# Kernel tuning notes

Measured on AMD Instinct MI355X. Metric: run time of the kernel, lower is better.

Reference implementation:

```python
import jax, jax.numpy as jnp
import numpy as np
from jax.scipy.linalg import solve_triangular

OMEGA = 1.5  # params_fix['omega']
BS, N, MAXITER = 512, 256, 200
RTOL = 1e-6


def setup_inputs() -> dict:
    key = jax.random.key(0)
    k1, k2, k3 = jax.random.split(key, 3)
    # diagonally dominant A so SOR converges
    A = jax.random.normal(k1, (BS, N, N), jnp.float32) + N * jnp.eye(N, dtype=jnp.float32)
    b = jax.random.normal(k2, (BS, N), jnp.float32)
    x_sol = jnp.linalg.solve(A, b[..., None])[..., 0]
    theta = jax.random.normal(k3, (BS, N), jnp.float32)  # initial iterate x0
    rtol = jnp.full((BS,), RTOL, jnp.float32)
    return {"A": A, "b": b, "x_sol": x_sol, "theta": theta, "rtol": rtol, "maxiter": MAXITER}


def reference(A, b, x_sol, theta, rtol, maxiter):
    bs, n, _ = A.shape
    b = b.reshape(bs, n, 1)
    x0 = theta.reshape(bs, n, 1)
    xs = x_sol.reshape(bs, n, 1)

    diag = jnp.diagonal(A, axis1=1, axis2=2)          # [bs, n]
    D = jnp.eye(n, dtype=A.dtype) * diag[:, :, None]  # diag_embed
    L = jnp.tril(A, -1)
    U = jnp.triu(A, 1)

    omega = jnp.asarray(OMEGA, A.dtype)
    G1 = D + omega * L                      # lower triangular, [bs, n, n]
    G2 = omega * U + (omega - 1.0) * D
    G = solve_triangular(G1, -G2, lower=True)        # iteration matrix
    f = solve_triangular(G1, omega * b, lower=True)  # affine term

    err0 = jnp.linalg.norm(xs - x0, axis=(1, 2))     # [bs]
    xtol = jnp.linalg.norm(xs, axis=(1, 2)) * rtol   # [bs]

    def step(carry, _):
        x, err, done = carry
        # global stopping criterion: while any(err > xtol)
        done = jnp.logical_or(done, jnp.logical_not(jnp.any(err > xtol)))
        x_new = jnp.where(done, x, G @ x + f)
        err_new = jnp.where(done, err, jnp.linalg.norm(xs - x_new, axis=(1, 2)))
        hist = jnp.where(done, jnp.zeros_like(err), err_new)  # unwritten slots stay 0
        return (x_new, err_new, done), hist

    init = (x0, err0, jnp.asarray(False))
    _, hist = jax.lax.scan(step, init, None, length=maxiter)  # hist: [maxiter, bs]
    return jnp.concatenate([err0[:, None], hist.T], axis=1)   # [bs, maxiter+1]
```

## Files before the change

kernel.cpp:

```cpp
#include <hip/hip_runtime.h>
#include <math.h>

#define BS 512
#define NN 256
#define RB 16
#define OMEGA_F 1.5f

__global__ __launch_bounds__(1024, 4) void sor_precompute(
    const float* __restrict__ A,
    const float* __restrict__ xs,
    const float* __restrict__ x0,
    const float* __restrict__ rtol,
    const int* __restrict__ maxiter_p,
    float* __restrict__ Gt,
    float* __restrict__ e0,
    float* __restrict__ err0_a,
    float* __restrict__ xtol_a,
    float* __restrict__ out)
{
    const int b   = blockIdx.x;
    const int tid = threadIdx.x;
    const int t   = tid & 255;
    const int q   = tid >> 8;
    const float* __restrict__ Ab  = A  + (size_t)b * NN * NN;
    float* __restrict__       Gtb = Gt + (size_t)b * NN * NN;

    __shared__ __align__(16) char smem[65536];
    float (*ldsA)[NN]     = (float (*)[NN])(smem);
    float (*acc2)[RB][NN] = (float (*)[RB][NN])(smem + 16384);
    float (*xbuf)[NN]     = (float (*)[NN])(smem + 49152);
    float* rs             = (float*)(smem + 16384);

    const int mi = *maxiter_p;

    if (q == 0) {
        const float xsv = xs[b * NN + t];
        const float ev  = xsv - x0[b * NN + t];
        e0[b * NN + t] = ev;
        float s1 = ev * ev, s2 = xsv * xsv;
        #pragma unroll
        for (int off = 32; off > 0; off >>= 1) {
            s1 += __shfl_down(s1, off);
            s2 += __shfl_down(s2, off);
        }
        if ((t & 63) == 0) { rs[t >> 6] = s1; rs[4 + (t >> 6)] = s2; }
    }
    __syncthreads();
    if (tid == 0) {
        const float S1 = rs[0] + rs[1] + rs[2] + rs[3];
        const float S2 = rs[4] + rs[5] + rs[6] + rs[7];
        const float er0 = sqrtf(S1);
        err0_a[b] = er0;
        xtol_a[b] = sqrtf(S2) * rtol[b];
        out[(size_t)b * (mi + 1)] = er0;
    }

    float g[4][RB];

    for (int KB = 0; KB < NN / RB; ++KB) {
        const int r0 = KB * RB;
        __syncthreads();
        {
            const int rr = tid >> 6;
            const int c  = (tid & 63) << 2;
            *(float4*)&ldsA[rr][c] = *(const float4*)&Ab[(size_t)(r0 + rr) * NN + c];
        }
        __syncthreads();

        float acc[RB];
        #pragma unroll
        for (int rr = 0; rr < RB; ++rr) acc[rr] = 0.f;
        #pragma unroll
        for (int m = 0; m < 4; ++m) {
            const int kbj = 4 * m + q;
            if (kbj < KB) {
                const int j0 = kbj * RB;
                #pragma unroll
                for (int jj4 = 0; jj4 < RB / 4; ++jj4) {
                    const float g0 = g[m][4 * jj4 + 0];
                    const float g1 = g[m][4 * jj4 + 1];
                    const float g2 = g[m][4 * jj4 + 2];
                    const float g3 = g[m][4 * jj4 + 3];
                    #pragma unroll
                    for (int rr = 0; rr < RB; ++rr) {
                        const float4 a4 = *(const float4*)&ldsA[rr][j0 + 4 * jj4];
                        acc[rr] += a4.x * g0 + a4.y * g1 + a4.z * g2 + a4.w * g3;
                    }
                }
            }
        }
        if (q < 2) {
            #pragma unroll
            for (int rr = 0; rr < RB; ++rr) acc2[q][rr][t] = acc[rr];
        }
        __syncthreads();
        if (q >= 2) {
            #pragma unroll
            for (int rr = 0; rr < RB; ++rr) acc2[q - 2][rr][t] += acc[rr];
        }
        __syncthreads();

        if (q == 0) {
            float s_[RB];
            #pragma unroll
            for (int rr = 0; rr < RB; ++rr)
                s_[rr] = acc2[0][rr][t] + acc2[1][rr][t];
            #pragma unroll
            for (int rr = 0; rr < RB; ++rr) {
                const int r = r0 + rr;
                const float a_rt = ldsA[rr][t];
                const float brt  = (t > r) ? (-OMEGA_F) * a_rt
                                 : ((t == r) ? (1.0f - OMEGA_F) * a_rt : 0.0f);
                const float diag = ldsA[rr][r];
                const float val  = (brt - OMEGA_F * s_[rr]) / diag;
                xbuf[rr][t] = val;
                Gtb[(size_t)t * NN + r] = val;
                #pragma unroll
                for (int rr2 = rr + 1; rr2 < RB; ++rr2)
                    s_[rr2] += ldsA[rr2][r] * val;
            }
        }
        __syncthreads();
        #pragma unroll
        for (int m = 0; m < 4; ++m) {
            if ((KB >> 2) == m && (KB & 3) == q) {
                #pragma unroll
                for (int rr = 0; rr < RB; ++rr) g[m][rr] = xbuf[rr][t];
            }
        }
    }
}

__global__ __launch_bounds__(1024, 4) void sor_iterate(
    const float* __restrict__ Gt,
    const float* __restrict__ e0,
    const float* __restrict__ err0_a,
    const float* __restrict__ xtol_a,
    const int* __restrict__ maxiter_p,
    float* __restrict__ out)
{
    const int b   = blockIdx.x;
    const int tid = threadIdx.x;
    const int w   = tid >> 6, u = tid & 63;
    const float* __restrict__ Gtb = Gt + (size_t)b * NN * NN;

    __shared__ __align__(16) float  e[NN];
    __shared__ __align__(16) float4 buf[16][64];
    __shared__ float errs_s;

    float4 g[16];
    #pragma unroll
    for (int jj = 0; jj < 16; ++jj)
        g[jj] = *(const float4*)&Gtb[(size_t)(16 * w + jj) * NN + 4 * u];

    if (tid < NN) e[tid] = e0[b * NN + tid];
    float err = err0_a[b];
    const float xtol = xtol_a[b];
    const int mi = *maxiter_p;
    float* __restrict__ outb = out + (size_t)b * (mi + 1);
    __syncthreads();

    int s = 1;
    for (; s <= mi; ++s) {
        if (!(err > xtol)) break;
        float4 acc = make_float4(0.f, 0.f, 0.f, 0.f);
        #pragma unroll
        for (int m = 0; m < 4; ++m) {
            const float4 ev = *(const float4*)&e[16 * w + 4 * m];
            acc.x += g[4*m+0].x*ev.x + g[4*m+1].x*ev.y + g[4*m+2].x*ev.z + g[4*m+3].x*ev.w;
            acc.y += g[4*m+0].y*ev.x + g[4*m+1].y*ev.y + g[4*m+2].y*ev.z + g[4*m+3].y*ev.w;
            acc.z += g[4*m+0].z*ev.x + g[4*m+1].z*ev.y + g[4*m+2].z*ev.z + g[4*m+3].z*ev.w;
            acc.w += g[4*m+0].w*ev.x + g[4*m+1].w*ev.y + g[4*m+2].w*ev.z + g[4*m+3].w*ev.w;
        }
        buf[w][u] = acc;
        __syncthreads();
        float4 p;
        if (w < 4) {
            const float4 p1 = buf[w + 4][u], p2 = buf[w + 8][u], p3 = buf[w + 12][u];
            p.x = acc.x + p1.x + p2.x + p3.x;
            p.y = acc.y + p1.y + p2.y + p3.y;
            p.z = acc.z + p1.z + p2.z + p3.z;
            p.w = acc.w + p1.w + p2.w + p3.w;
            if (w) buf[w][u] = p;
        }
        __syncthreads();
        if (w == 0) {
            const float4 b1 = buf[1][u], b2 = buf[2][u], b3 = buf[3][u];
            float4 r;
            r.x = p.x + b1.x + b2.x + b3.x;
            r.y = p.y + b1.y + b2.y + b3.y;
            r.z = p.z + b1.z + b2.z + b3.z;
            r.w = p.w + b1.w + b2.w + b3.w;
            *(float4*)&e[4 * u] = r;
            float loc = r.x * r.x + r.y * r.y + r.z * r.z + r.w * r.w;
            #pragma unroll
            for (int off = 32; off > 0; off >>= 1) loc += __shfl_down(loc, off);
            if (u == 0) {
                const float er = sqrtf(loc);
                errs_s = er;
                outb[s] = er;
            }
        }
        __syncthreads();
        err = errs_s;
    }
    for (int idx = s + tid; idx <= mi; idx += 1024) outb[idx] = 0.f;
}

extern "C" void kernel_launch(void* const* d_in, const int* in_sizes, int n_in,
                              void* d_out, int out_size, void* d_ws, size_t ws_size,
                              hipStream_t stream) {
    const float* A     = (const float*)d_in[0];
    const float* xs    = (const float*)d_in[2];
    const float* theta = (const float*)d_in[3];
    const float* rtol  = (const float*)d_in[4];
    const int*   mi    = (const int*)d_in[5];
    float* out = (float*)d_out;

    float* Gt   = (float*)d_ws;
    float* e0   = Gt + (size_t)BS * NN * NN;
    float* err0 = e0 + (size_t)BS * NN;
    float* xtol = err0 + BS;

    sor_precompute<<<dim3(BS), dim3(1024), 0, stream>>>(
        A, xs, theta, rtol, mi, Gt, e0, err0, xtol, out);
    sor_iterate<<<dim3(BS), dim3(1024), 0, stream>>>(
        Gt, e0, err0, xtol, mi, out);
}
```

Baseline: 661.0 us.

## Fuse SOR precompute and iteration kernels, keeping iteration matrix in registers

Merges the triangular-solve precompute and the SOR iteration loop into one kernel. The iteration matrix G is redistributed from the solve's register layout into the iteration layout through a skewed LDS transpose, so it is never written to or read back from global memory. The inner triangular-solve product now reads A directly from global/L1 instead of the LDS tile, and the wave-uniform branch index is forced scalar with readfirstlane. This removes a launch and a large global round trip of G, at the cost of register pressure, extra LDS transposes and possibly slower direct global reads of A.

```diff
diff --git a/kernel.cpp b/kernel.cpp
--- a/kernel.cpp
+++ b/kernel.cpp
@@ -6,37 +6,40 @@
 #define RB 16
 #define OMEGA_F 1.5f
 
-__global__ __launch_bounds__(1024, 4) void sor_precompute(
+__global__ __launch_bounds__(1024, 4) void sor_fused(
     const float* __restrict__ A,
     const float* __restrict__ xs,
     const float* __restrict__ x0,
     const float* __restrict__ rtol,
     const int* __restrict__ maxiter_p,
-    float* __restrict__ Gt,
-    float* __restrict__ e0,
-    float* __restrict__ err0_a,
-    float* __restrict__ xtol_a,
     float* __restrict__ out)
 {
     const int b   = blockIdx.x;
     const int tid = threadIdx.x;
     const int t   = tid & 255;
     const int q   = tid >> 8;
-    const float* __restrict__ Ab  = A  + (size_t)b * NN * NN;
-    float* __restrict__       Gtb = Gt + (size_t)b * NN * NN;
+    const int qU  = __builtin_amdgcn_readfirstlane(q);
+    const int w   = tid >> 6;
+    const int u   = tid & 63;
+    const float* __restrict__ Ab = A + (size_t)b * NN * NN;
 
     __shared__ __align__(16) char smem[65536];
     float (*ldsA)[NN]     = (float (*)[NN])(smem);
     float (*acc2)[RB][NN] = (float (*)[RB][NN])(smem + 16384);
     float (*xbuf)[NN]     = (float (*)[NN])(smem + 49152);
+    float (*ldsX)[NN]     = (float (*)[NN])(smem);
     float* rs             = (float*)(smem + 16384);
+    float* e              = (float*)(smem);
+    float4 (*buf)[64]     = (float4 (*)[64])(smem + 1024);
+    float* errs_p         = (float*)(smem + 17408);
 
     const int mi = *maxiter_p;
-
+    float* __restrict__ outb = out + (size_t)b * (mi + 1);
+
+    float ev = 0.f;
     if (q == 0) {
         const float xsv = xs[b * NN + t];
-        const float ev  = xsv - x0[b * NN + t];
-        e0[b * NN + t] = ev;
+        ev = xsv - x0[b * NN + t];
         float s1 = ev * ev, s2 = xsv * xsv;
         #pragma unroll
         for (int off = 32; off > 0; off >>= 1) {
@@ -46,17 +49,11 @@
         if ((t & 63) == 0) { rs[t >> 6] = s1; rs[4 + (t >> 6)] = s2; }
     }
     __syncthreads();
-    if (tid == 0) {
-        const float S1 = rs[0] + rs[1] + rs[2] + rs[3];
-        const float S2 = rs[4] + rs[5] + rs[6] + rs[7];
-        const float er0 = sqrtf(S1);
-        err0_a[b] = er0;
-        xtol_a[b] = sqrtf(S2) * rtol[b];
-        out[(size_t)b * (mi + 1)] = er0;
-    }
+    const float err0 = sqrtf(rs[0] + rs[1] + rs[2] + rs[3]);
+    const float xtol = sqrtf(rs[4] + rs[5] + rs[6] + rs[7]) * rtol[b];
+    if (tid == 0) outb[0] = err0;
 
     float g[4][RB];
-
     for (int KB = 0; KB < NN / RB; ++KB) {
         const int r0 = KB * RB;
         __syncthreads();
@@ -72,23 +69,30 @@
         for (int rr = 0; rr < RB; ++rr) acc[rr] = 0.f;
         #pragma unroll
         for (int m = 0; m < 4; ++m) {
-            const int kbj = 4 * m + q;
+            const int kbj = 4 * m + qU;
             if (kbj < KB) {
                 const int j0 = kbj * RB;
                 #pragma unroll
-                for (int jj4 = 0; jj4 < RB / 4; ++jj4) {
-                    const float g0 = g[m][4 * jj4 + 0];
-                    const float g1 = g[m][4 * jj4 + 1];
-                    const float g2 = g[m][4 * jj4 + 2];
-                    const float g3 = g[m][4 * jj4 + 3];
+                for (int jw = 0; jw < 4; ++jw) {
+                    const float g0 = g[m][4 * jw + 0];
+                    const float g1 = g[m][4 * jw + 1];
+                    const float g2 = g[m][4 * jw + 2];
+                    const float g3 = g[m][4 * jw + 3];
                     #pragma unroll
-                    for (int rr = 0; rr < RB; ++rr) {
-                        const float4 a4 = *(const float4*)&ldsA[rr][j0 + 4 * jj4];
-                        acc[rr] += a4.x * g0 + a4.y * g1 + a4.z * g2 + a4.w * g3;
+                    for (int hc = 0; hc < 4; ++hc) {
+                        float4 a_[4];
+                        #pragma unroll
+                        for (int h = 0; h < 4; ++h)
+                            a_[h] = *(const float4*)&Ab[(size_t)(r0 + 4 * hc + h) * NN + j0 + 4 * jw];
+                        #pragma unroll
+                        for (int h = 0; h < 4; ++h)
+                            acc[4 * hc + h] += a_[h].x * g0 + a_[h].y * g1
+                                             + a_[h].z * g2 + a_[h].w * g3;
                     }
                 }
             }
         }
+
         if (q < 2) {
             #pragma unroll
             for (int rr = 0; rr < RB; ++rr) acc2[q][rr][t] = acc[rr];
@@ -114,7 +118,6 @@
                 const float diag = ldsA[rr][r];
                 const float val  = (brt - OMEGA_F * s_[rr]) / diag;
                 xbuf[rr][t] = val;
-                Gtb[(size_t)t * NN + r] = val;
                 #pragma unroll
                 for (int rr2 = rr + 1; rr2 < RB; ++rr2)
                     s_[rr2] += ldsA[rr2][r] * val;
@@ -129,58 +132,58 @@
             }
         }
     }
-}
-
-__global__ __launch_bounds__(1024, 4) void sor_iterate(
-    const float* __restrict__ Gt,
-    const float* __restrict__ e0,
-    const float* __restrict__ err0_a,
-    const float* __restrict__ xtol_a,
-    const int* __restrict__ maxiter_p,
-    float* __restrict__ out)
-{
-    const int b   = blockIdx.x;
-    const int tid = threadIdx.x;
-    const int w   = tid >> 6, u = tid & 63;
-    const float* __restrict__ Gtb = Gt + (size_t)b * NN * NN;
-
-    __shared__ __align__(16) float  e[NN];
-    __shared__ __align__(16) float4 buf[16][64];
-    __shared__ float errs_s;
-
-    float4 g[16];
+
+    float4 gi[16];
     #pragma unroll
-    for (int jj = 0; jj < 16; ++jj)
-        g[jj] = *(const float4*)&Gtb[(size_t)(16 * w + jj) * NN + 4 * u];
-
-    if (tid < NN) e[tid] = e0[b * NN + tid];
-    float err = err0_a[b];
-    const float xtol = xtol_a[b];
-    const int mi = *maxiter_p;
-    float* __restrict__ outb = out + (size_t)b * (mi + 1);
+    for (int R = 0; R < 4; ++R) {
+        __syncthreads();
+        #pragma unroll
+        for (int rr = 0; rr < RB; ++rr) {
+            const int lr = q * RB + rr;
+            ldsX[lr][(t + lr) & 255] = g[R][rr];
+        }
+        __syncthreads();
+        if ((u >> 4) == R) {
+            #pragma unroll
+            for (int jj = 0; jj < 16; ++jj) {
+                const int tcol = 16 * w + jj;
+                float vx[4];
+                #pragma unroll
+                for (int c = 0; c < 4; ++c) {
+                    const int lr = 4 * (u & 15) + c;
+                    vx[c] = ldsX[lr][(tcol + lr) & 255];
+                }
+                gi[jj] = make_float4(vx[0], vx[1], vx[2], vx[3]);
+            }
+        }
+    }
     __syncthreads();
 
+    if (tid < NN) e[tid] = ev;
+    __syncthreads();
+
+    float err = err0;
     int s = 1;
     for (; s <= mi; ++s) {
         if (!(err > xtol)) break;
-        float4 acc = make_float4(0.f, 0.f, 0.f, 0.f);
+        float4 acc4 = make_float4(0.f, 0.f, 0.f, 0.f);
         #pragma unroll
         for (int m = 0; m < 4; ++m) {
-            const float4 ev = *(const float4*)&e[16 * w + 4 * m];
-            acc.x += g[4*m+0].x*ev.x + g[4*m+1].x*ev.y + g[4*m+2].x*ev.z + g[4*m+3].x*ev.w;
-            acc.y += g[4*m+0].y*ev.x + g[4*m+1].y*ev.y + g[4*m+2].y*ev.z + g[4*m+3].y*ev.w;
-            acc.z += g[4*m+0].z*ev.x + g[4*m+1].z*ev.y + g[4*m+2].z*ev.z + g[4*m+3].z*ev.w;
-            acc.w += g[4*m+0].w*ev.x + g[4*m+1].w*ev.y + g[4*m+2].w*ev.z + g[4*m+3].w*ev.w;
-        }
-        buf[w][u] = acc;
+            const float4 evv = *(const float4*)&e[16 * w + 4 * m];
+            acc4.x += gi[4*m+0].x*evv.x + gi[4*m+1].x*evv.y + gi[4*m+2].x*evv.z + gi[4*m+3].x*evv.w;
+            acc4.y += gi[4*m+0].y*evv.x + gi[4*m+1].y*evv.y + gi[4*m+2].y*evv.z + gi[4*m+3].y*evv.w;
+            acc4.z += gi[4*m+0].z*evv.x + gi[4*m+1].z*evv.y + gi[4*m+2].z*evv.z + gi[4*m+3].z*evv.w;
+            acc4.w += gi[4*m+0].w*evv.x + gi[4*m+1].w*evv.y + gi[4*m+2].w*evv.z + gi[4*m+3].w*evv.w;
+        }
+        buf[w][u] = acc4;
         __syncthreads();
         float4 p;
         if (w < 4) {
             const float4 p1 = buf[w + 4][u], p2 = buf[w + 8][u], p3 = buf[w + 12][u];
-            p.x = acc.x + p1.x + p2.x + p3.x;
-            p.y = acc.y + p1.y + p2.y + p3.y;
-            p.z = acc.z + p1.z + p2.z + p3.z;
-            p.w = acc.w + p1.w + p2.w + p3.w;
+            p.x = acc4.x + p1.x + p2.x + p3.x;
+            p.y = acc4.y + p1.y + p2.y + p3.y;
+            p.z = acc4.z + p1.z + p2.z + p3.z;
+            p.w = acc4.w + p1.w + p2.w + p3.w;
             if (w) buf[w][u] = p;
         }
         __syncthreads();
@@ -197,12 +200,12 @@
             for (int off = 32; off > 0; off >>= 1) loc += __shfl_down(loc, off);
             if (u == 0) {
                 const float er = sqrtf(loc);
-                errs_s = er;
+                *errs_p = er;
                 outb[s] = er;
             }
         }
         __syncthreads();
-        err = errs_s;
+        err = *errs_p;
     }
     for (int idx = s + tid; idx <= mi; idx += 1024) outb[idx] = 0.f;
 }
@@ -217,13 +220,6 @@
     const int*   mi    = (const int*)d_in[5];
     float* out = (float*)d_out;
 
-    float* Gt   = (float*)d_ws;
-    float* e0   = Gt + (size_t)BS * NN * NN;
-    float* err0 = e0 + (size_t)BS * NN;
-    float* xtol = err0 + BS;
-
-    sor_precompute<<<dim3(BS), dim3(1024), 0, stream>>>(
-        A, xs, theta, rtol, mi, Gt, e0, err0, xtol, out);
-    sor_iterate<<<dim3(BS), dim3(1024), 0, stream>>>(
-        Gt, e0, err0, xtol, mi, out);
+    sor_fused<<<dim3(BS), dim3(1024), 0, stream>>>(
+        A, xs, theta, rtol, mi, out);
 }
```

Measured after the change: 698.6 us. +5.7%, slower.
